# Performance work log

Hardware: AMD Instinct MI355X
Metric: run time of the kernel (lower is better)

Reference implementation:

```python
import jax, jax.numpy as jnp
import numpy as np

BS, L, D = 2048, 32, 768
KS = 5  # gaussian kernel size
EPS = 1e-5


def layer_norm(x, g, b):
    m = x.mean(-1, keepdims=True)
    var = ((x - m) ** 2).mean(-1, keepdims=True)
    return (x - m) * jax.lax.rsqrt(var + EPS) * g + b


def setup_inputs() -> dict:
    key = jax.random.key(0)
    ks = jax.random.split(key, 12)
    s = 0.02
    return {
        "v": jax.random.normal(ks[0], (BS, L, D), jnp.float32),
        "qa": jax.random.normal(ks[1], (BS, D), jnp.float32),
        # v_proj: LayerNorm -> Linear(D,D) -> GELU
        "vp_lng": jnp.ones((D,), jnp.float32),
        "vp_lnb": jnp.zeros((D,), jnp.float32),
        "vp_w": jax.random.normal(ks[2], (D, D), jnp.float32) * s,
        "vp_b": jnp.zeros((D,), jnp.float32),
        # qa_proj: LayerNorm -> Linear(D,D) -> GELU
        "qp_lng": jnp.ones((D,), jnp.float32),
        "qp_lnb": jnp.zeros((D,), jnp.float32),
        "qp_w": jax.random.normal(ks[3], (D, D), jnp.float32) * s,
        "qp_b": jnp.zeros((D,), jnp.float32),
        # grounding: LayerNorm -> Linear(D,D/2) -> GELU -> Linear(D/2,1) -> Softmax(dim=-2)
        "g_lng": jnp.ones((D,), jnp.float32),
        "g_lnb": jnp.zeros((D,), jnp.float32),
        "g_w1": jax.random.normal(ks[4], (D, D // 2), jnp.float32) * s,
        "g_b1": jnp.zeros((D // 2,), jnp.float32),
        "g_w2": jax.random.normal(ks[5], (D // 2, 1), jnp.float32) * s,
        "g_b2": jnp.zeros((1,), jnp.float32),
        # adaptive gaussian filter sigma (scalar parameter, initial 1.0)
        "sigma": jnp.array(1.0, jnp.float32),
    }


def reference(v, qa, vp_lng, vp_lnb, vp_w, vp_b, qp_lng, qp_lnb, qp_w, qp_b,
              g_lng, g_lnb, g_w1, g_b1, g_w2, g_b2, sigma):
    bs, length = v.shape[0], v.shape[1]
    # projections (exact erf GELU, matching torch nn.GELU default)
    v_p = jax.nn.gelu(layer_norm(v, vp_lng, vp_lnb) @ vp_w + vp_b, approximate=False)
    qa_p = jax.nn.gelu(layer_norm(qa, qp_lng, qp_lnb) @ qp_w + qp_b, approximate=False)
    # gate = tanh(v @ qa) : [bs, L, 1]
    gate = jnp.tanh(jnp.einsum('bld,bd->bl', v_p, qa_p))[..., None]
    # grounding head -> softmax over frames
    h = layer_norm(v_p * gate, g_lng, g_lnb)
    h = jax.nn.gelu(h @ g_w1 + g_b1, approximate=False)
    logits = h @ g_w2 + g_b2                      # [bs, L, 1]
    ori_key = jax.nn.softmax(logits, axis=1)[..., 0]  # [bs, L]
    # adaptive gaussian smoothing (depthwise conv1d, symmetric 5-tap kernel) + softmax
    xk = jnp.arange(KS, dtype=jnp.float32) - KS // 2
    kern = jnp.exp(-0.5 * (xk / sigma) ** 2)
    kern = kern / kern.sum()
    xp = jnp.pad(ori_key, ((0, 0), (KS // 2, KS // 2)))
    taps = jnp.stack([xp[:, k:k + length] for k in range(KS)], axis=0)  # [KS, bs, L]
    smoothed = jnp.einsum('k,kbl->bl', kern, taps)
    key_gs = jax.nn.softmax(smoothed, axis=1)         # [bs, L]
    # find_best_interval_v2, vectorized: among windows of size {1,3,5} that
    # contain the (first) argmax frame, pick the window with highest prob-sum;
    # ties resolve to smallest window then earliest start (strict > in loop ==
    # first occurrence of the max in (w, start) order == jnp.argmax semantics).
    pmax = jnp.argmax(key_gs, axis=1)                 # [bs]
    cum = jnp.pad(jnp.cumsum(key_gs, axis=1), ((0, 0), (1, 0)))
    scores_all, starts_all, ends_all = [], [], []
    for w in (1, 3, 5):
        s = jnp.arange(length - w + 1)
        sums = cum[:, s + w] - cum[:, s]              # sliding window sums
        contains = (pmax[:, None] >= s[None, :]) & (pmax[:, None] < s[None, :] + w)
        scores_all.append(jnp.where(contains, sums, -jnp.inf))
        starts_all.append(s)
        ends_all.append(s + w)                        # NOTE: exclusive end stored, as in original
    scores = jnp.concatenate(scores_all, axis=1)
    starts = jnp.concatenate(starts_all)
    ends = jnp.concatenate(ends_all)
    idx = jnp.argmax(scores, axis=1)
    st = starts[idx]
    en = ends[idx]
    max_indices = jnp.stack([st, en], axis=1)         # [bs, 2]
    rng = jnp.arange(length)
    mask = (rng[None, :] >= st[:, None]) & (rng[None, :] <= en[:, None])
    start_time = st.astype(jnp.float32) / 31.0
    end_time = en.astype(jnp.float32) / 31.0
    return key_gs, max_indices, start_time, end_time, mask, ori_key
```

## Files before the change

### kernel.cpp

```cpp
#include <hip/hip_runtime.h>
#include <math.h>
#include <stdint.h>


#define DEV __device__ __forceinline__

typedef __attribute__((ext_vector_type(8))) short short8v;
typedef __attribute__((ext_vector_type(4))) float f32x4;

constexpr int KDIM  = 768;
constexpr int CHUNK = 32768;

constexpr int OFF_KG   = 0;
constexpr int OFF_MI   = 65536;
constexpr int OFF_ST   = 69632;
constexpr int OFF_ET   = 71680;
constexpr int OFF_MASK = 73728;
constexpr int OFF_ORI  = 139264;

DEV float wave_sum(float v) { for (int o = 32; o; o >>= 1) v += __shfl_xor(v, o); return v; }
DEV float wave_max(float v) { for (int o = 32; o; o >>= 1) v = fmaxf(v, __shfl_xor(v, o)); return v; }

DEV float gelu_fast(float x) {
    float z = x * 0.70710678118654752f;
    float s = fabsf(z);
    float t = __builtin_amdgcn_rcpf(fmaf(0.3275911f, s, 1.0f));
    float p = t * fmaf(t, fmaf(t, fmaf(t, fmaf(t, 1.061405429f, -1.453152027f),
                                       1.421413741f), -0.284496736f), 0.254829592f);
    float e = __expf(-s * s);
    float er = copysignf(1.0f - p * e, z);
    return 0.5f * x * (1.0f + er);
}

DEV short f2bf(float x) {
    uint32_t u = __builtin_bit_cast(uint32_t, x);
    u = u + 0x7fffu + ((u >> 16) & 1u);
    return (short)(u >> 16);
}
DEV float bf2f(short b) {
    uint32_t u = ((uint32_t)(uint16_t)b) << 16;
    return __builtin_bit_cast(float, u);
}
DEV float asf(uint32_t u) { return __builtin_bit_cast(float, u); }

DEV void gl_lds16(const void* g, void* l) {
    __builtin_amdgcn_global_load_lds(
        (const __attribute__((address_space(1))) uint32_t*)g,
        (__attribute__((address_space(3))) uint32_t*)l, 16, 0, 0);
}

__global__ __launch_bounds__(256)
void prep_A1(const float* __restrict__ X, const float* __restrict__ g,
             const float* __restrict__ b, short* __restrict__ Ah, short* __restrict__ Al)
{
    int w = threadIdx.x >> 6, lane = threadIdx.x & 63;
    int row = blockIdx.x * 4 + w;
    const float4* xr = (const float4*)(X + (size_t)row * KDIM);
    float4 xv[3]; float s = 0.f, ss = 0.f;
#pragma unroll
    for (int i = 0; i < 3; ++i) {
        xv[i] = xr[lane + i * 64];
        s  += xv[i].x + xv[i].y + xv[i].z + xv[i].w;
        ss += xv[i].x * xv[i].x + xv[i].y * xv[i].y + xv[i].z * xv[i].z + xv[i].w * xv[i].w;
    }
    s = wave_sum(s); ss = wave_sum(ss);
    float m = s * (1.f / 768.f), var = ss * (1.f / 768.f) - m * m;
    float sa = rsqrtf(var + 1e-5f), ta = -m * sa;
#pragma unroll
    for (int i = 0; i < 3; ++i) {
        int idx = lane + i * 64;
        float4 gv = ((const float4*)g)[idx];
        float4 bv = ((const float4*)b)[idx];
        float a0 = fmaf(fmaf(xv[i].x, sa, ta), gv.x, bv.x);
        float a1 = fmaf(fmaf(xv[i].y, sa, ta), gv.y, bv.y);
        float a2 = fmaf(fmaf(xv[i].z, sa, ta), gv.z, bv.z);
        float a3 = fmaf(fmaf(xv[i].w, sa, ta), gv.w, bv.w);
        short h0 = f2bf(a0), h1 = f2bf(a1), h2 = f2bf(a2), h3 = f2bf(a3);
        ushort4 hv, lv;
        hv.x = (uint16_t)h0; hv.y = (uint16_t)h1; hv.z = (uint16_t)h2; hv.w = (uint16_t)h3;
        lv.x = (uint16_t)f2bf(a0 - bf2f(h0)); lv.y = (uint16_t)f2bf(a1 - bf2f(h1));
        lv.z = (uint16_t)f2bf(a2 - bf2f(h2)); lv.w = (uint16_t)f2bf(a3 - bf2f(h3));
        ((ushort4*)(Ah + (size_t)row * KDIM))[idx] = hv;
        ((ushort4*)(Al + (size_t)row * KDIM))[idx] = lv;
    }
}

__global__ __launch_bounds__(256)
void prep_A2(const uint32_t* __restrict__ vp_hl, const float* __restrict__ qa_p,
             const float* __restrict__ g, const float* __restrict__ b,
             short* __restrict__ Ah, short* __restrict__ Al, int chunk_off)
{
    int w = threadIdx.x >> 6, lane = threadIdx.x & 63;
    int row = blockIdx.x * 4 + w;
    int bidx = (chunk_off + row) >> 5;
    const uint4*  hr = (const uint4*)(vp_hl + (size_t)row * KDIM);
    const float4* qr = (const float4*)(qa_p + (size_t)bidx * KDIM);
    float vp[12]; float s = 0.f, ss = 0.f, d = 0.f;
#pragma unroll
    for (int i = 0; i < 3; ++i) {
        uint4  uv = hr[lane + i * 64];
        float4 qv = qr[lane + i * 64];
        float v0 = asf(uv.x & 0xffff0000u) + asf(uv.x << 16);
        float v1 = asf(uv.y & 0xffff0000u) + asf(uv.y << 16);
        float v2 = asf(uv.z & 0xffff0000u) + asf(uv.z << 16);
        float v3 = asf(uv.w & 0xffff0000u) + asf(uv.w << 16);
        vp[i * 4 + 0] = v0; vp[i * 4 + 1] = v1; vp[i * 4 + 2] = v2; vp[i * 4 + 3] = v3;
        s  += v0 + v1 + v2 + v3;
        ss += v0 * v0 + v1 * v1 + v2 * v2 + v3 * v3;
        d  += v0 * qv.x + v1 * qv.y + v2 * qv.z + v3 * qv.w;
    }
    s = wave_sum(s); ss = wave_sum(ss); d = wave_sum(d);
    float gate = tanhf(d);
    float m = s * (1.f / 768.f), var = ss * (1.f / 768.f) - m * m;
    float den = rsqrtf(gate * gate * var + 1e-5f);
    float sa = gate * den, ta = -gate * m * den;
#pragma unroll
    for (int i = 0; i < 3; ++i) {
        int idx = lane + i * 64;
        float4 gv = ((const float4*)g)[idx];
        float4 bv = ((const float4*)b)[idx];
        float a0 = fmaf(fmaf(vp[i * 4 + 0], sa, ta), gv.x, bv.x);
        float a1 = fmaf(fmaf(vp[i * 4 + 1], sa, ta), gv.y, bv.y);
        float a2 = fmaf(fmaf(vp[i * 4 + 2], sa, ta), gv.z, bv.z);
        float a3 = fmaf(fmaf(vp[i * 4 + 3], sa, ta), gv.w, bv.w);
        short h0 = f2bf(a0), h1 = f2bf(a1), h2 = f2bf(a2), h3 = f2bf(a3);
        ushort4 hv, lv;
        hv.x = (uint16_t)h0; hv.y = (uint16_t)h1; hv.z = (uint16_t)h2; hv.w = (uint16_t)h3;
        lv.x = (uint16_t)f2bf(a0 - bf2f(h0)); lv.y = (uint16_t)f2bf(a1 - bf2f(h1));
        lv.z = (uint16_t)f2bf(a2 - bf2f(h2)); lv.w = (uint16_t)f2bf(a3 - bf2f(h3));
        ((ushort4*)(Ah + (size_t)row * KDIM))[idx] = hv;
        ((ushort4*)(Al + (size_t)row * KDIM))[idx] = lv;
    }
}

__global__ __launch_bounds__(256)
void prep_W(const float* __restrict__ W, short* __restrict__ Bh, short* __restrict__ Bl, int N)
{
    __shared__ float t[32][33];
    int bx = blockIdx.x, by = blockIdx.y;
    int lx = threadIdx.x & 31, ly = threadIdx.x >> 5;
#pragma unroll
    for (int r = 0; r < 32; r += 8)
        t[ly + r][lx] = W[(size_t)(by * 32 + ly + r) * N + bx * 32 + lx];
    __syncthreads();
#pragma unroll
    for (int r = 0; r < 32; r += 8) {
        float v = t[lx][ly + r];
        short hi = f2bf(v);
        size_t o = (size_t)(bx * 32 + ly + r) * KDIM + by * 32 + lx;
        Bh[o] = hi;
        Bl[o] = f2bf(v - bf2f(hi));
    }
}

#define VMW(N_) asm volatile("s_waitcnt vmcnt(" #N_ ")" ::: "memory")

#define STG(G_, KT_) gl_lds16(sp[G_] + (KT_) * 32,                            \
    lds + (((KT_) & 1) ? BUFSZ : 0) + (G_) * 4096 + toff)

#define RDA(dst, BOFF) do {                                                   \
    _Pragma("unroll")                                                         \
    for (int mf = 0; mf < 4; ++mf) {                                          \
        int rA = wm * 64 + mf * 16 + lr;                                      \
        dst[mf] = *(const short8v*)(bb + (BOFF) + rA * 64 +                   \
                                    ((lh ^ ((rA >> 1) & 3)) << 4));           \
    } } while (0)

#define RDB(dst, BOFF) do {                                                   \
    _Pragma("unroll")                                                         \
    for (int nf = 0; nf < 4; ++nf) {                                          \
        int rB = wn * 64 + nf * 16 + lr;                                      \
        dst[nf] = *(const short8v*)(bb + (BOFF) + rB * 64 +                   \
                                    ((lh ^ ((rB >> 1) & 3)) << 4));           \
    } } while (0)

#define SYNCMM(aop, bop) do {                                                 \
    __builtin_amdgcn_sched_barrier(0);                                        \
    __builtin_amdgcn_s_barrier();                                             \
    asm volatile("s_waitcnt lgkmcnt(0)" ::: "memory");                        \
    __builtin_amdgcn_sched_barrier(0);                                        \
    __builtin_amdgcn_s_setprio(1);                                            \
    _Pragma("unroll")                                                         \
    for (int mf = 0; mf < 4; ++mf)                                            \
        _Pragma("unroll")                                                     \
        for (int nf = 0; nf < 4; ++nf)                                        \
            acc[mf][nf] = __builtin_amdgcn_mfma_f32_16x16x32_bf16(            \
                aop[mf], bop[nf], acc[mf][nf], 0, 0, 0);                      \
    __builtin_amdgcn_s_setprio(0);                                            \
    __builtin_amdgcn_sched_barrier(0);                                        \
    __builtin_amdgcn_s_barrier();                                             \
    } while (0)

template<int MODE>
__global__ __launch_bounds__(256, 2)
void gemm8(const short* __restrict__ Ah_g, const short* __restrict__ Al_g,
           const short* __restrict__ Bh_g, const short* __restrict__ Bl_g,
           const float* __restrict__ bias, uint32_t* __restrict__ O_hl,
           const float* __restrict__ w2, float* __restrict__ partials,
           int chunk_off)
{
    constexpr int BUFSZ = 32768;
    extern __shared__ __align__(16) char lds[];

    const int t = threadIdx.x;
    const int w = t >> 6, lane = t & 63;
    const int lr = lane & 15, lh = lane >> 4;
    const int wm = w >> 1, wn = w & 1;

    const int gx = gridDim.x, nwg = gx * gridDim.y;
    int bidx = blockIdx.y * gx + blockIdx.x;
    int wid = (bidx & 7) * (nwg >> 3) + (bidx >> 3);
    const int bx = wid % gx, by = wid / gx;
    const int row0 = by * 128, col0 = bx * 128;

    const int r_ = t >> 2, c_ = t & 3;
    const int swz_ = (c_ ^ ((r_ >> 1) & 3)) << 3;
    const int toff = t * 16;
    const short* sp[8];
    sp[0] = Ah_g + (size_t)(row0 + r_)      * KDIM + swz_;
    sp[1] = Ah_g + (size_t)(row0 + 64 + r_) * KDIM + swz_;
    sp[2] = Bh_g + (size_t)(col0 + r_)      * KDIM + swz_;
    sp[3] = Bh_g + (size_t)(col0 + 64 + r_) * KDIM + swz_;
    sp[4] = Bl_g + (size_t)(col0 + r_)      * KDIM + swz_;
    sp[5] = Bl_g + (size_t)(col0 + 64 + r_) * KDIM + swz_;
    sp[6] = Al_g + (size_t)(row0 + r_)      * KDIM + swz_;
    sp[7] = Al_g + (size_t)(row0 + 64 + r_) * KDIM + swz_;

    f32x4 acc[4][4] = {};
    short8v ah[4], al[4], bh[4], bl[4];

    STG(0, 0); STG(1, 0); STG(2, 0); STG(3, 0);
    STG(4, 0); STG(5, 0); STG(6, 0); STG(7, 0);
    VMW(4);
    __builtin_amdgcn_s_barrier();

    for (int kt = 0; kt < 24; ++kt) {
        const char* bb = lds + ((kt & 1) ? BUFSZ : 0);
        const bool nl = (kt < 23);
        RDA(ah, 0); RDB(bh, 8192);
        if (nl) { STG(0, kt + 1); STG(1, kt + 1); STG(2, kt + 1); VMW(4); }
        else    { VMW(2); }
        SYNCMM(ah, bh);
        RDB(bl, 16384);
        if (nl) { STG(3, kt + 1); STG(4, kt + 1); STG(5, kt + 1); VMW(6); }
        else    { VMW(0); }
        SYNCMM(ah, bl);
        RDA(al, 24576);
        if (nl) { STG(6, kt + 1); STG(7, kt + 1); VMW(4); }
        SYNCMM(al, bh);
    }

    if (MODE == 0) {
#pragma unroll
        for (int mf = 0; mf < 4; ++mf)
#pragma unroll
            for (int nf = 0; nf < 4; ++nf) {
                int n = col0 + wn * 64 + nf * 16 + lr;
                float bvs = bias[n];
#pragma unroll
                for (int q = 0; q < 4; ++q) {
                    int m = row0 + wm * 64 + mf * 16 + lh * 4 + q;
                    float gv = gelu_fast(acc[mf][nf][q] + bvs);
                    uint32_t u  = __builtin_bit_cast(uint32_t, gv);
                    uint32_t hb = u & 0xffff0000u;
                    float rem   = gv - asf(hb);
                    O_hl[(size_t)m * 768 + n] =
                        hb | (uint32_t)(uint16_t)f2bf(rem);
                }
            }
    } else {
        float rs[4][4] = {};
#pragma unroll
        for (int mf = 0; mf < 4; ++mf)
#pragma unroll
            for (int nf = 0; nf < 4; ++nf) {
                int n = col0 + wn * 64 + nf * 16 + lr;
                float bvs = bias[n], wv = w2[n];
#pragma unroll
                for (int q = 0; q < 4; ++q)
                    rs[mf][q] += gelu_fast(acc[mf][nf][q] + bvs) * wv;
            }
#pragma unroll
        for (int mf = 0; mf < 4; ++mf)
#pragma unroll
            for (int q = 0; q < 4; ++q) {
                float vv = rs[mf][q];
                vv += __shfl_xor(vv, 1); vv += __shfl_xor(vv, 2);
                vv += __shfl_xor(vv, 4); vv += __shfl_xor(vv, 8);
                if (lr == 0) {
                    int m = chunk_off + row0 + wm * 64 + mf * 16 + lh * 4 + q;
                    partials[(size_t)(bx * 2 + wn) * 65536 + m] = vv;
                }
            }
    }
}

constexpr int BKF = 16;
__global__ __launch_bounds__(256)
void rowstats(const float* __restrict__ X, float2* __restrict__ st, int M)
{
    int wave = threadIdx.x >> 6, lane = threadIdx.x & 63;
    int row = blockIdx.x * 4 + wave;
    if (row >= M) return;
    const float4* xr = reinterpret_cast<const float4*>(X + (size_t)row * KDIM);
    float s = 0.f, ss = 0.f;
#pragma unroll
    for (int i = 0; i < 3; ++i) {
        float4 v = xr[lane + i * 64];
        s  += v.x + v.y + v.z + v.w;
        ss += v.x * v.x + v.y * v.y + v.z * v.z + v.w * v.w;
    }
    s = wave_sum(s); ss = wave_sum(ss);
    if (lane == 0) {
        float m = s * (1.0f / 768.0f);
        float var = ss * (1.0f / 768.0f) - m * m;
        float rstd = rsqrtf(var + 1e-5f);
        st[row] = make_float2(rstd, -m * rstd);
    }
}

template<int BM, int BN, int TM, int TN>
__global__ __launch_bounds__(256)
void gemm_fused(const float* __restrict__ X, const float2* __restrict__ st,
                const float* __restrict__ gw, const float* __restrict__ gb,
                const float* __restrict__ W, const float* __restrict__ bias,
                float* __restrict__ out, int M, int N)
{
    static_assert((BM / TM) * (BN / TN) == 256, "256 threads");
    __shared__ float As[BKF][BM];
    __shared__ float Bs[BKF][BN];
    const int t = threadIdx.x;
    constexpr int TXN = BN / TN;
    const int tx = t % TXN;
    const int ty = t / TXN;
    const int row0 = blockIdx.y * BM;
    const int col0 = blockIdx.x * BN;
    float acc[TM][TN] = {};
    constexpr int A_IT = BM * BKF / 4 / 256;
    constexpr int B_IT = BKF * BN / 4 / 256;
    for (int k0 = 0; k0 < KDIM; k0 += BKF) {
#pragma unroll
        for (int i = 0; i < A_IT; ++i) {
            int idx = t + i * 256;
            int r = idx >> 2;
            int c = (idx & 3) << 2;
            float4 xv = *reinterpret_cast<const float4*>(X + (size_t)(row0 + r) * KDIM + k0 + c);
            float2 s = st[row0 + r];
            float4 gv = *reinterpret_cast<const float4*>(gw + k0 + c);
            float4 bv = *reinterpret_cast<const float4*>(gb + k0 + c);
            As[c + 0][r] = fmaf(fmaf(xv.x, s.x, s.y), gv.x, bv.x);
            As[c + 1][r] = fmaf(fmaf(xv.y, s.x, s.y), gv.y, bv.y);
            As[c + 2][r] = fmaf(fmaf(xv.z, s.x, s.y), gv.z, bv.z);
            As[c + 3][r] = fmaf(fmaf(xv.w, s.x, s.y), gv.w, bv.w);
        }
#pragma unroll
        for (int i = 0; i < B_IT; ++i) {
            int idx = t + i * 256;
            int r = idx / (BN / 4);
            int c = (idx % (BN / 4)) << 2;
            *reinterpret_cast<float4*>(&Bs[r][c]) =
                *reinterpret_cast<const float4*>(W + (size_t)(k0 + r) * N + col0 + c);
        }
        __syncthreads();
#pragma unroll
        for (int kk = 0; kk < BKF; ++kk) {
            float a[TM], b[TN];
#pragma unroll
            for (int i = 0; i < TM; i += 4)
                *reinterpret_cast<float4*>(&a[i]) = *reinterpret_cast<const float4*>(&As[kk][ty * TM + i]);
#pragma unroll
            for (int j = 0; j < TN; j += 4)
                *reinterpret_cast<float4*>(&b[j]) = *reinterpret_cast<const float4*>(&Bs[kk][tx * TN + j]);
#pragma unroll
            for (int i = 0; i < TM; ++i)
#pragma unroll
                for (int j = 0; j < TN; ++j)
                    acc[i][j] = fmaf(a[i], b[j], acc[i][j]);
        }
        __syncthreads();
    }
#pragma unroll
    for (int i = 0; i < TM; ++i) {
        size_t row = row0 + ty * TM + i;
#pragma unroll
        for (int j = 0; j < TN; j += 4) {
            int col = col0 + tx * TN + j;
            float4 o;
            o.x = gelu_fast(acc[i][j + 0] + bias[col + 0]);
            o.y = gelu_fast(acc[i][j + 1] + bias[col + 1]);
            o.z = gelu_fast(acc[i][j + 2] + bias[col + 2]);
            o.w = gelu_fast(acc[i][j + 3] + bias[col + 3]);
            *reinterpret_cast<float4*>(out + row * N + col) = o;
        }
    }
}

__global__ __launch_bounds__(64)
void head_kernel(const float* __restrict__ partials, const float* __restrict__ b2,
                 const float* __restrict__ sigma_p, float* __restrict__ out)
{
    int b = blockIdx.x, lane = threadIdx.x;
    __shared__ float ok[36];
    __shared__ float kg[32];
    __shared__ int sel[2];

    if (lane < 36) ok[lane] = 0.f;
    __syncthreads();

    float x = -3.4e38f;
    if (lane < 32) {
        int row = b * 32 + lane;
        x = b2[0];
#pragma unroll
        for (int p = 0; p < 6; ++p) x += partials[(size_t)p * 65536 + row];
    }
    float mx = wave_max(x);
    float e = (lane < 32) ? expf(x - mx) : 0.f;
    float sum = wave_sum(e);
    float ori = e / sum;
    if (lane < 32) {
        out[OFF_ORI + b * 32 + lane] = ori;
        ok[lane + 2] = ori;
    }
    __syncthreads();

    float sg = sigma_p[0];
    float kern[5]; float ks = 0.f;
#pragma unroll
    for (int k = 0; k < 5; ++k) { float xx = (float)(k - 2) / sg; kern[k] = expf(-0.5f * xx * xx); ks += kern[k]; }
    float sm = -3.4e38f;
    if (lane < 32) {
        sm = 0.f;
#pragma unroll
        for (int k = 0; k < 5; ++k) sm += (kern[k] / ks) * ok[lane + k];
    }
    float mx2 = wave_max(sm);
    float e2 = (lane < 32) ? expf(sm - mx2) : 0.f;
    float sum2 = wave_sum(e2);
    float kgv = e2 / sum2;
    if (lane < 32) {
        out[OFF_KG + b * 32 + lane] = kgv;
        kg[lane] = kgv;
    }
    __syncthreads();

    if (lane == 0) {
        int pm = 0; float bv = kg[0];
        for (int i = 1; i < 32; ++i) if (kg[i] > bv) { bv = kg[i]; pm = i; }
        float cum[33]; cum[0] = 0.f;
        for (int i = 0; i < 32; ++i) cum[i + 1] = cum[i] + kg[i];
        float bs = -3.4e38f; int bst = 0, ben = 0;
        const int wsz[3] = {1, 3, 5};
        for (int wi = 0; wi < 3; ++wi) {
            int w = wsz[wi];
            for (int s = 0; s + w <= 32; ++s) {
                if (pm >= s && pm < s + w) {
                    float sc = cum[s + w] - cum[s];
                    if (sc > bs) { bs = sc; bst = s; ben = s + w; }
                }
            }
        }
        out[OFF_MI + b * 2 + 0] = (float)bst;
        out[OFF_MI + b * 2 + 1] = (float)ben;
        out[OFF_ST + b] = (float)bst / 31.0f;
        out[OFF_ET + b] = (float)ben / 31.0f;
        sel[0] = bst; sel[1] = ben;
    }
    __syncthreads();
    if (lane < 32)
        out[OFF_MASK + b * 32 + lane] = (lane >= sel[0] && lane <= sel[1]) ? 1.0f : 0.0f;
}

extern "C" void kernel_launch(void* const* d_in, const int* in_sizes, int n_in,
                              void* d_out, int out_size, void* d_ws, size_t ws_size,
                              hipStream_t stream)
{
    const float* v      = (const float*)d_in[0];
    const float* qa     = (const float*)d_in[1];
    const float* vp_lng = (const float*)d_in[2];
    const float* vp_lnb = (const float*)d_in[3];
    const float* vp_w   = (const float*)d_in[4];
    const float* vp_b   = (const float*)d_in[5];
    const float* qp_lng = (const float*)d_in[6];
    const float* qp_lnb = (const float*)d_in[7];
    const float* qp_w   = (const float*)d_in[8];
    const float* qp_b   = (const float*)d_in[9];
    const float* g_lng  = (const float*)d_in[10];
    const float* g_lnb  = (const float*)d_in[11];
    const float* g_w1   = (const float*)d_in[12];
    const float* g_b1   = (const float*)d_in[13];
    const float* g_w2   = (const float*)d_in[14];
    const float* g_b2   = (const float*)d_in[15];
    const float* sigma  = (const float*)d_in[16];
    float* outf = (float*)d_out;

    short* A1h = (short*)d_ws;
    short* A1l = A1h + (size_t)CHUNK * KDIM;
    uint32_t* vp_hl = (uint32_t*)(A1l + (size_t)CHUNK * KDIM);
    short* B1h = (short*)(vp_hl + (size_t)CHUNK * KDIM);
    short* B1l = B1h + 768 * KDIM;
    short* B2h = B1l + 768 * KDIM;
    short* B2l = B2h + 384 * KDIM;
    float* qa_p = (float*)(B2l + 384 * KDIM);
    float* st_qa = qa_p + 2048 * KDIM;
    float* partials = st_qa + 4096;

    rowstats<<<512, 256, 0, stream>>>(qa, (float2*)st_qa, 2048);
    gemm_fused<64, 64, 4, 4><<<dim3(12, 32), 256, 0, stream>>>(
        qa, (const float2*)st_qa, qp_lng, qp_lnb, qp_w, qp_b, qa_p, 2048, 768);

    prep_W<<<dim3(24, 24), 256, 0, stream>>>(vp_w, B1h, B1l, 768);
    prep_W<<<dim3(12, 24), 256, 0, stream>>>(g_w1, B2h, B2l, 384);

    constexpr int LDS8 = 65536;

    for (int c = 0; c < 65536; c += CHUNK) {
        prep_A1<<<CHUNK / 4, 256, 0, stream>>>(v + (size_t)c * KDIM, vp_lng, vp_lnb, A1h, A1l);
        gemm8<0><<<dim3(6, CHUNK / 128), 256, LDS8, stream>>>(
            A1h, A1l, B1h, B1l, vp_b, vp_hl, nullptr, nullptr, 0);
        prep_A2<<<CHUNK / 4, 256, 0, stream>>>(vp_hl, qa_p, g_lng, g_lnb, A1h, A1l, c);
        gemm8<1><<<dim3(3, CHUNK / 128), 256, LDS8, stream>>>(
            A1h, A1l, B2h, B2l, g_b1, nullptr, g_w2, partials, c);
    }

    head_kernel<<<2048, 64, 0, stream>>>(partials, g_b2, sigma, outf);
}
```

Baseline: 562.5 us.

## Load B operands directly from global into registers, stage only A in LDS

```diff
diff --git a/kernel.cpp b/kernel.cpp
--- a/kernel.cpp
+++ b/kernel.cpp
@@ -154,42 +154,51 @@
 }
 
 #define VMW(N_) asm volatile("s_waitcnt vmcnt(" #N_ ")" ::: "memory")
-
-#define STG(G_, KT_) gl_lds16(sp[G_] + (KT_) * 32,                            \
-    lds + (((KT_) & 1) ? BUFSZ : 0) + (G_) * 4096 + toff)
-
-#define RDA(dst, BOFF) do {                                                   \
-    _Pragma("unroll")                                                         \
+#define SCB __builtin_amdgcn_sched_barrier(0)
+
+#define STGA(KT_) do { char* db_ = lds + (((KT_) & 1) ? BUFSZ : 0);           \
+    gl_lds16(sa[0] + (KT_) * 32, db_ + toff);                                 \
+    gl_lds16(sa[1] + (KT_) * 32, db_ + 4096 + toff);                          \
+    gl_lds16(sa[2] + (KT_) * 32, db_ + 8192 + toff);                          \
+    gl_lds16(sa[3] + (KT_) * 32, db_ + 12288 + toff); } while (0)
+
+#define LOADB(DST, KT_) do { _Pragma("unroll")                                \
+    for (int j_ = 0; j_ < 8; ++j_)                                            \
+        DST[j_] = *(const short8v*)(bp[j_] + (KT_) * 32); } while (0)
+
+#define RDA(dst, BOFF) do { _Pragma("unroll")                                 \
     for (int mf = 0; mf < 4; ++mf) {                                          \
         int rA = wm * 64 + mf * 16 + lr;                                      \
         dst[mf] = *(const short8v*)(bb + (BOFF) + rA * 64 +                   \
                                     ((lh ^ ((rA >> 1) & 3)) << 4));           \
     } } while (0)
 
-#define RDB(dst, BOFF) do {                                                   \
-    _Pragma("unroll")                                                         \
-    for (int nf = 0; nf < 4; ++nf) {                                          \
-        int rB = wn * 64 + nf * 16 + lr;                                      \
-        dst[nf] = *(const short8v*)(bb + (BOFF) + rB * 64 +                   \
-                                    ((lh ^ ((rB >> 1) & 3)) << 4));           \
-    } } while (0)
-
-#define SYNCMM(aop, bop) do {                                                 \
-    __builtin_amdgcn_sched_barrier(0);                                        \
-    __builtin_amdgcn_s_barrier();                                             \
+#define BODY(KT_, BCUR, BNXT, NL_) do {                                       \
+    const char* bb = lds + (((KT_) & 1) ? BUFSZ : 0);                         \
+    RDA(ah, 0); RDA(al, 8192);                                                \
+    if (NL_) { STGA((KT_) + 1); }                                             \
+    SCB;                                                                      \
+    if (NL_) { LOADB(BNXT, (KT_) + 1); }                                      \
+    SCB;                                                                      \
+    if (NL_) { VMW(12); } else { VMW(0); }                                    \
     asm volatile("s_waitcnt lgkmcnt(0)" ::: "memory");                        \
-    __builtin_amdgcn_sched_barrier(0);                                        \
+    SCB;                                                                      \
     __builtin_amdgcn_s_setprio(1);                                            \
     _Pragma("unroll")                                                         \
     for (int mf = 0; mf < 4; ++mf)                                            \
         _Pragma("unroll")                                                     \
-        for (int nf = 0; nf < 4; ++nf)                                        \
+        for (int nf = 0; nf < 4; ++nf) {                                      \
             acc[mf][nf] = __builtin_amdgcn_mfma_f32_16x16x32_bf16(            \
-                aop[mf], bop[nf], acc[mf][nf], 0, 0, 0);                      \
+                ah[mf], BCUR[nf], acc[mf][nf], 0, 0, 0);                      \
+            acc[mf][nf] = __builtin_amdgcn_mfma_f32_16x16x32_bf16(            \
+                ah[mf], BCUR[4 + nf], acc[mf][nf], 0, 0, 0);                  \
+            acc[mf][nf] = __builtin_amdgcn_mfma_f32_16x16x32_bf16(            \
+                al[mf], BCUR[nf], acc[mf][nf], 0, 0, 0);                      \
+        }                                                                     \
     __builtin_amdgcn_s_setprio(0);                                            \
-    __builtin_amdgcn_sched_barrier(0);                                        \
-    __builtin_amdgcn_s_barrier();                                             \
-    } while (0)
+    SCB;                                                                      \
+    if (NL_) { VMW(8); __builtin_amdgcn_s_barrier(); }                        \
+} while (0)
 
 template<int MODE>
 __global__ __launch_bounds__(256, 2)
@@ -199,7 +208,7 @@
            const float* __restrict__ w2, float* __restrict__ partials,
            int chunk_off)
 {
-    constexpr int BUFSZ = 32768;
+    constexpr int BUFSZ = 16384;
     extern __shared__ __align__(16) char lds[];
 
     const int t = threadIdx.x;
@@ -216,38 +225,34 @@
     const int r_ = t >> 2, c_ = t & 3;
     const int swz_ = (c_ ^ ((r_ >> 1) & 3)) << 3;
     const int toff = t * 16;
-    const short* sp[8];
-    sp[0] = Ah_g + (size_t)(row0 + r_)      * KDIM + swz_;
-    sp[1] = Ah_g + (size_t)(row0 + 64 + r_) * KDIM + swz_;
-    sp[2] = Bh_g + (size_t)(col0 + r_)      * KDIM + swz_;
-    sp[3] = Bh_g + (size_t)(col0 + 64 + r_) * KDIM + swz_;
-    sp[4] = Bl_g + (size_t)(col0 + r_)      * KDIM + swz_;
-    sp[5] = Bl_g + (size_t)(col0 + 64 + r_) * KDIM + swz_;
-    sp[6] = Al_g + (size_t)(row0 + r_)      * KDIM + swz_;
-    sp[7] = Al_g + (size_t)(row0 + 64 + r_) * KDIM + swz_;
+    const short* sa[4];
+    sa[0] = Ah_g + (size_t)(row0 + r_)      * KDIM + swz_;
+    sa[1] = Ah_g + (size_t)(row0 + 64 + r_) * KDIM + swz_;
+    sa[2] = Al_g + (size_t)(row0 + r_)      * KDIM + swz_;
+    sa[3] = Al_g + (size_t)(row0 + 64 + r_) * KDIM + swz_;
+
+    const short* bp[8];
+#pragma unroll
+    for (int nf = 0; nf < 4; ++nf) {
+        int n = col0 + wn * 64 + nf * 16 + lr;
+        bp[nf]     = Bh_g + (size_t)n * KDIM + lh * 8;
+        bp[4 + nf] = Bl_g + (size_t)n * KDIM + lh * 8;
+    }
 
     f32x4 acc[4][4] = {};
-    short8v ah[4], al[4], bh[4], bl[4];
-
-    STG(0, 0); STG(1, 0); STG(2, 0); STG(3, 0);
-    STG(4, 0); STG(5, 0); STG(6, 0); STG(7, 0);
-    VMW(4);
+    short8v ah[4], al[4];
+    short8v bA[8], bB[8];
+
+    STGA(0);
+    SCB;
+    LOADB(bA, 0);
+    SCB;
+    VMW(8);
     __builtin_amdgcn_s_barrier();
 
-    for (int kt = 0; kt < 24; ++kt) {
-        const char* bb = lds + ((kt & 1) ? BUFSZ : 0);
-        const bool nl = (kt < 23);
-        RDA(ah, 0); RDB(bh, 8192);
-        if (nl) { STG(0, kt + 1); STG(1, kt + 1); STG(2, kt + 1); VMW(4); }
-        else    { VMW(2); }
-        SYNCMM(ah, bh);
-        RDB(bl, 16384);
-        if (nl) { STG(3, kt + 1); STG(4, kt + 1); STG(5, kt + 1); VMW(6); }
-        else    { VMW(0); }
-        SYNCMM(ah, bl);
-        RDA(al, 24576);
-        if (nl) { STG(6, kt + 1); STG(7, kt + 1); VMW(4); }
-        SYNCMM(al, bh);
+    for (int kt = 0; kt < 24; kt += 2) {
+        BODY(kt,     bA, bB, true);
+        BODY(kt + 1, bB, bA, (kt + 1 < 23));
     }
 
     if (MODE == 0) {
@@ -512,7 +517,7 @@
     prep_W<<<dim3(24, 24), 256, 0, stream>>>(vp_w, B1h, B1l, 768);
     prep_W<<<dim3(12, 24), 256, 0, stream>>>(g_w1, B2h, B2l, 384);
 
-    constexpr int LDS8 = 65536;
+    constexpr int LDS8 = 32768;
 
     for (int c = 0; c < 65536; c += CHUNK) {
         prep_A1<<<CHUNK / 4, 256, 0, stream>>>(v + (size_t)c * KDIM, vp_lng, vp_lnb, A1h, A1l);
```

Result: slower. 747.6 us (+32.9%).

## Restructure split-bf16 GEMM mainloop: issue full next-tile prefetch, then fused MFMA block

Applied to the files above, without the earlier changes.

```diff
diff --git a/kernel.cpp b/kernel.cpp
--- a/kernel.cpp
+++ b/kernel.cpp
@@ -154,42 +154,54 @@
 }
 
 #define VMW(N_) asm volatile("s_waitcnt vmcnt(" #N_ ")" ::: "memory")
+#define SCB __builtin_amdgcn_sched_barrier(0)
 
 #define STG(G_, KT_) gl_lds16(sp[G_] + (KT_) * 32,                            \
     lds + (((KT_) & 1) ? BUFSZ : 0) + (G_) * 4096 + toff)
 
-#define RDA(dst, BOFF) do {                                                   \
-    _Pragma("unroll")                                                         \
+#define STGA8(KT_) do { STG(0, KT_); STG(1, KT_); STG(2, KT_); STG(3, KT_);   \
+    STG(4, KT_); STG(5, KT_); STG(6, KT_); STG(7, KT_); } while (0)
+
+#define RDA(dst, BOFF) do { _Pragma("unroll")                                 \
     for (int mf = 0; mf < 4; ++mf) {                                          \
         int rA = wm * 64 + mf * 16 + lr;                                      \
         dst[mf] = *(const short8v*)(bb + (BOFF) + rA * 64 +                   \
                                     ((lh ^ ((rA >> 1) & 3)) << 4));           \
     } } while (0)
 
-#define RDB(dst, BOFF) do {                                                   \
-    _Pragma("unroll")                                                         \
+#define RDB(dst, BOFF) do { _Pragma("unroll")                                 \
     for (int nf = 0; nf < 4; ++nf) {                                          \
         int rB = wn * 64 + nf * 16 + lr;                                      \
         dst[nf] = *(const short8v*)(bb + (BOFF) + rB * 64 +                   \
                                     ((lh ^ ((rB >> 1) & 3)) << 4));           \
     } } while (0)
 
-#define SYNCMM(aop, bop) do {                                                 \
-    __builtin_amdgcn_sched_barrier(0);                                        \
-    __builtin_amdgcn_s_barrier();                                             \
+#define BODY(KT_, NL_) do {                                                   \
+    if (NL_) { STGA8((KT_) + 1); }                                            \
+    SCB;                                                                      \
+    if (NL_) { VMW(8); } else { VMW(0); }                                     \
+    SCB;                                                                      \
+    __builtin_amdgcn_s_barrier();             \
+    const char* bb = lds + (((KT_) & 1) ? BUFSZ : 0);                         \
+    RDA(ah, 0); RDB(bh, 8192); RDB(bl, 16384); RDA(al, 24576);                \
     asm volatile("s_waitcnt lgkmcnt(0)" ::: "memory");                        \
-    __builtin_amdgcn_sched_barrier(0);                                        \
+    SCB;                                                                      \
+    __builtin_amdgcn_s_barrier();                  \
     __builtin_amdgcn_s_setprio(1);                                            \
     _Pragma("unroll")                                                         \
     for (int mf = 0; mf < 4; ++mf)                                            \
         _Pragma("unroll")                                                     \
-        for (int nf = 0; nf < 4; ++nf)                                        \
+        for (int nf = 0; nf < 4; ++nf) {                                      \
             acc[mf][nf] = __builtin_amdgcn_mfma_f32_16x16x32_bf16(            \
-                aop[mf], bop[nf], acc[mf][nf], 0, 0, 0);                      \
+                ah[mf], bh[nf], acc[mf][nf], 0, 0, 0);                        \
+            acc[mf][nf] = __builtin_amdgcn_mfma_f32_16x16x32_bf16(            \
+                ah[mf], bl[nf], acc[mf][nf], 0, 0, 0);                        \
+            acc[mf][nf] = __builtin_amdgcn_mfma_f32_16x16x32_bf16(            \
+                al[mf], bh[nf], acc[mf][nf], 0, 0, 0);                        \
+        }                                                                     \
     __builtin_amdgcn_s_setprio(0);                                            \
-    __builtin_amdgcn_sched_barrier(0);                                        \
-    __builtin_amdgcn_s_barrier();                                             \
-    } while (0)
+    SCB;                                                                      \
+} while (0)
 
 template<int MODE>
 __global__ __launch_bounds__(256, 2)
@@ -229,25 +241,12 @@
     f32x4 acc[4][4] = {};
     short8v ah[4], al[4], bh[4], bl[4];
 
-    STG(0, 0); STG(1, 0); STG(2, 0); STG(3, 0);
-    STG(4, 0); STG(5, 0); STG(6, 0); STG(7, 0);
-    VMW(4);
-    __builtin_amdgcn_s_barrier();
-
-    for (int kt = 0; kt < 24; ++kt) {
-        const char* bb = lds + ((kt & 1) ? BUFSZ : 0);
-        const bool nl = (kt < 23);
-        RDA(ah, 0); RDB(bh, 8192);
-        if (nl) { STG(0, kt + 1); STG(1, kt + 1); STG(2, kt + 1); VMW(4); }
-        else    { VMW(2); }
-        SYNCMM(ah, bh);
-        RDB(bl, 16384);
-        if (nl) { STG(3, kt + 1); STG(4, kt + 1); STG(5, kt + 1); VMW(6); }
-        else    { VMW(0); }
-        SYNCMM(ah, bl);
-        RDA(al, 24576);
-        if (nl) { STG(6, kt + 1); STG(7, kt + 1); VMW(4); }
-        SYNCMM(al, bh);
+    STGA8(0);
+    SCB;
+
+    for (int kt = 0; kt < 24; kt += 2) {
+        BODY(kt,     true);
+        BODY(kt + 1, (kt + 1 < 23));
     }
 
     if (MODE == 0) {
```

After: 559.6 us. No clear change (-0.5%).
